# Kernel tuning notes

Hardware: AMD Instinct MI355X
Metric: run time of the kernel (lower is better)

## Reference

```python
import jax, jax.numpy as jnp
import numpy as np


def _wkv(time_decay, time_first, k, v):
    # time_decay, time_first: [C]; k, v: [B, T, C]
    w = -jnp.exp(time_decay)  # per-channel decay (negative)
    u = time_first
    B, T, C = k.shape
    aa = jnp.zeros((B, C), dtype=k.dtype)
    bb = jnp.zeros((B, C), dtype=k.dtype)
    pp = jnp.full((B, C), -1e38, dtype=k.dtype)  # running max exponent

    def step(carry, kv_t):
        aa, bb, pp = carry
        kt, vt = kv_t  # [B, C] each
        # output with bonus u for current token
        ww = u + kt
        q = jnp.maximum(pp, ww)
        e1 = jnp.exp(pp - q)
        e2 = jnp.exp(ww - q)
        y_t = (e1 * aa + e2 * vt) / (e1 * bb + e2)
        # decayed state update
        ww2 = pp + w
        q2 = jnp.maximum(ww2, kt)
        e1b = jnp.exp(ww2 - q2)
        e2b = jnp.exp(kt - q2)
        new_carry = (e1b * aa + e2b * vt, e1b * bb + e2b, q2)
        return new_carry, y_t

    ks = jnp.transpose(k, (1, 0, 2))  # [T, B, C]
    vs = jnp.transpose(v, (1, 0, 2))
    _, ys = jax.lax.scan(step, (aa, bb, pp), (ks, vs))
    return jnp.transpose(ys, (1, 0, 2))  # [B, T, C]


def setup_inputs() -> dict:
    key = jax.random.key(0)
    k1, k2, k3, k4 = jax.random.split(key, 4)
    B, T, C = 8, 1024, 2048
    return {
        "batch_size": B,
        "seq_len": T,
        "embedding_dim": C,
        "time_decay": jax.random.normal(k1, (C,), dtype=jnp.float32),
        "time_first": jax.random.normal(k2, (C,), dtype=jnp.float32),
        "k": jax.random.normal(k3, (B, T, C), dtype=jnp.float32),
        "v": jax.random.normal(k4, (B, T, C), dtype=jnp.float32),
    }


def reference(batch_size, seq_len, embedding_dim, time_decay, time_first, k, v):
    assert seq_len <= 1024  # T_max
    return _wkv(time_decay, time_first, k, v)
```

## Files before the change

kernel.cpp:

```cpp
#include <hip/hip_runtime.h>


#define T_FIX  1024
#define NCH    64
#define CHL    (T_FIX / NCH)
#define BATCH  8
#define SBATCH 8
#define L2E    1.4426950408889634f

__device__ __forceinline__ void wkv_step2(float& aa, float& bb, float& pp,
                                          float w2, float k2, float vt)
{
    float ww2 = pp + w2;
    float q2  = fmaxf(ww2, k2);
    float e1  = exp2f(ww2 - q2);
    float e2  = exp2f(k2 - q2);
    aa = fmaf(e1, aa, e2 * vt);
    bb = fmaf(e1, bb, e2);
    pp = q2;
}

#define F4TOA(a, f) { a[0] = (f).x; a[1] = (f).y; a[2] = (f).z; a[3] = (f).w; }

__global__ __launch_bounds__(256)
void wkv_states(const float* __restrict__ td,
                const float* __restrict__ k,
                const float* __restrict__ v,
                float* __restrict__ aa_s,
                float* __restrict__ bb_s,
                float* __restrict__ pp_s,
                int B, int C)
{
    const int C4  = C >> 2;
    int gid = blockIdx.x * blockDim.x + threadIdx.x;
    if (gid >= B * NCH * C4) return;
    int c4  = gid % C4;
    int rem = gid / C4;
    int j   = rem % NCH;
    int b   = rem / NCH;
    int c   = c4 << 2;

    float4 tdv = *(const float4*)(td + c);
    float w2[4] = { -__expf(tdv.x) * L2E, -__expf(tdv.y) * L2E,
                    -__expf(tdv.z) * L2E, -__expf(tdv.w) * L2E };

    const size_t base = ((size_t)b * T_FIX + (size_t)j * CHL) * C + c;
    const float* kp = k + base;
    const float* vp = v + base;

    float aa[4] = {0.f, 0.f, 0.f, 0.f};
    float bb[4] = {0.f, 0.f, 0.f, 0.f};
    float pp[4] = {-1e38f, -1e38f, -1e38f, -1e38f};

    for (int tb = 0; tb < CHL; tb += BATCH) {
        float4 kb[BATCH], vb[BATCH];
        #pragma unroll
        for (int i = 0; i < BATCH; ++i) {
            kb[i] = *(const float4*)(kp + (size_t)(tb + i) * C);
            vb[i] = *(const float4*)(vp + (size_t)(tb + i) * C);
        }
        #pragma unroll
        for (int i = 0; i < BATCH; ++i) {
            float ka[4], va[4];
            F4TOA(ka, kb[i]); F4TOA(va, vb[i]);
            #pragma unroll
            for (int cc = 0; cc < 4; ++cc)
                wkv_step2(aa[cc], bb[cc], pp[cc], w2[cc], ka[cc] * L2E, va[cc]);
        }
    }

    size_t sidx = ((size_t)j * B + b) * C + c;
    *(float4*)(aa_s + sidx) = make_float4(aa[0], aa[1], aa[2], aa[3]);
    *(float4*)(bb_s + sidx) = make_float4(bb[0], bb[1], bb[2], bb[3]);
    *(float4*)(pp_s + sidx) = make_float4(pp[0], pp[1], pp[2], pp[3]);
}

__global__ __launch_bounds__(256)
void wkv_scan(const float* __restrict__ td,
              float* __restrict__ aa_s,
              float* __restrict__ bb_s,
              float* __restrict__ pp_s,
              int B, int C)
{
    const int C4 = C >> 2;
    int gid = blockIdx.x * blockDim.x + threadIdx.x;
    if (gid >= B * C4) return;
    int c4 = gid % C4;
    int b  = gid / C4;
    int c  = c4 << 2;

    float4 tdv = *(const float4*)(td + c);
    float wL[4] = { -__expf(tdv.x) * (L2E * (float)CHL),
                    -__expf(tdv.y) * (L2E * (float)CHL),
                    -__expf(tdv.z) * (L2E * (float)CHL),
                    -__expf(tdv.w) * (L2E * (float)CHL) };

    float aa[4] = {0.f, 0.f, 0.f, 0.f};
    float bb[4] = {0.f, 0.f, 0.f, 0.f};
    float pp[4] = {-1e38f, -1e38f, -1e38f, -1e38f};

    for (int jb = 0; jb < NCH; jb += SBATCH) {
        float4 ca4[SBATCH], cb4[SBATCH], cm4[SBATCH];
        #pragma unroll
        for (int i = 0; i < SBATCH; ++i) {
            size_t sidx = ((size_t)(jb + i) * B + b) * C + c;
            ca4[i] = *(const float4*)(aa_s + sidx);
            cb4[i] = *(const float4*)(bb_s + sidx);
            cm4[i] = *(const float4*)(pp_s + sidx);
        }
        #pragma unroll
        for (int i = 0; i < SBATCH; ++i) {
            size_t sidx = ((size_t)(jb + i) * B + b) * C + c;
            *(float4*)(aa_s + sidx) = make_float4(aa[0], aa[1], aa[2], aa[3]);
            *(float4*)(bb_s + sidx) = make_float4(bb[0], bb[1], bb[2], bb[3]);
            *(float4*)(pp_s + sidx) = make_float4(pp[0], pp[1], pp[2], pp[3]);
            float ca[4], cb[4], cm[4];
            F4TOA(ca, ca4[i]); F4TOA(cb, cb4[i]); F4TOA(cm, cm4[i]);
            #pragma unroll
            for (int cc = 0; cc < 4; ++cc) {
                float ppd = pp[cc] + wL[cc];
                float pn  = fmaxf(ppd, cm[cc]);
                float ea  = exp2f(ppd - pn);
                float eb  = exp2f(cm[cc] - pn);
                aa[cc] = fmaf(ea, aa[cc], eb * ca[cc]);
                bb[cc] = fmaf(ea, bb[cc], eb * cb[cc]);
                pp[cc] = pn;
            }
        }
    }
}

__global__ __launch_bounds__(256)
void wkv_emit(const float* __restrict__ td,
              const float* __restrict__ tf,
              const float* __restrict__ k,
              const float* __restrict__ v,
              const float* __restrict__ aa_s,
              const float* __restrict__ bb_s,
              const float* __restrict__ pp_s,
              float* __restrict__ y,
              int B, int C)
{
    const int C4  = C >> 2;
    int gid = blockIdx.x * blockDim.x + threadIdx.x;
    if (gid >= B * NCH * C4) return;
    int c4  = gid % C4;
    int rem = gid / C4;
    int j   = rem % NCH;
    int b   = rem / NCH;
    int c   = c4 << 2;

    float4 tdv = *(const float4*)(td + c);
    float4 tfv = *(const float4*)(tf + c);
    float w2[4] = { -__expf(tdv.x) * L2E, -__expf(tdv.y) * L2E,
                    -__expf(tdv.z) * L2E, -__expf(tdv.w) * L2E };
    float u2[4] = { tfv.x * L2E, tfv.y * L2E, tfv.z * L2E, tfv.w * L2E };

    size_t sidx = ((size_t)j * B + b) * C + c;
    float4 a4 = *(const float4*)(aa_s + sidx);
    float4 b4 = *(const float4*)(bb_s + sidx);
    float4 p4 = *(const float4*)(pp_s + sidx);
    float aa[4], bb[4], pp[4];
    F4TOA(aa, a4); F4TOA(bb, b4); F4TOA(pp, p4);

    const size_t base = ((size_t)b * T_FIX + (size_t)j * CHL) * C + c;
    const float* kp = k + base;
    const float* vp = v + base;
    float*       yp = y + base;

    for (int tb = 0; tb < CHL; tb += BATCH) {
        float4 kb[BATCH], vb[BATCH];
        #pragma unroll
        for (int i = 0; i < BATCH; ++i) {
            kb[i] = *(const float4*)(kp + (size_t)(tb + i) * C);
            vb[i] = *(const float4*)(vp + (size_t)(tb + i) * C);
        }
        #pragma unroll
        for (int i = 0; i < BATCH; ++i) {
            float ka[4], va[4], ya[4];
            F4TOA(ka, kb[i]); F4TOA(va, vb[i]);
            #pragma unroll
            for (int cc = 0; cc < 4; ++cc) {
                float k2 = ka[cc] * L2E;
                float ww = u2[cc] + k2;
                float q  = fmaxf(pp[cc], ww);
                float e1 = exp2f(pp[cc] - q);
                float e2 = exp2f(ww - q);
                ya[cc] = __fdividef(fmaf(e1, aa[cc], e2 * va[cc]),
                                    fmaf(e1, bb[cc], e2));
                wkv_step2(aa[cc], bb[cc], pp[cc], w2[cc], k2, va[cc]);
            }
            *(float4*)(yp + (size_t)(tb + i) * C) = make_float4(ya[0], ya[1], ya[2], ya[3]);
        }
    }
}

extern "C" void kernel_launch(void* const* d_in, const int* in_sizes, int n_in,
                              void* d_out, int out_size, void* d_ws, size_t ws_size,
                              hipStream_t stream)
{
    const float* td = (const float*)d_in[3];
    const float* tf = (const float*)d_in[4];
    const float* k  = (const float*)d_in[5];
    const float* v  = (const float*)d_in[6];
    float*       y  = (float*)d_out;

    const int C   = in_sizes[3];
    const int BTC = in_sizes[5];
    const int B   = BTC / (T_FIX * C);

    const size_t N = (size_t)B * C * NCH;
    float* aa_s = (float*)d_ws;
    float* bb_s = aa_s + N;
    float* pp_s = bb_s + N;

    const int block = 256;

    const int threadsA = B * NCH * (C >> 2);
    const int gridA    = (threadsA + block - 1) / block;

    const int threadsS = B * (C >> 2);
    const int gridS    = (threadsS + block - 1) / block;

    wkv_states<<<gridA, block, 0, stream>>>(td, k, v, aa_s, bb_s, pp_s, B, C);
    wkv_scan  <<<gridS, block, 0, stream>>>(td, aa_s, bb_s, pp_s, B, C);
    wkv_emit  <<<gridA, block, 0, stream>>>(td, tf, k, v, aa_s, bb_s, pp_s, y, B, C);
}
```

Measured before the change: 232.0 us.

## Fuse chunked WKV into one kernel with in-block shared-memory prefix scan

Merges the three kernels (chunk states, serial cross-chunk scan, emit) into one. Each 512-thread block owns one batch and a 32-channel tile across all 64 time chunks. The chunk states go into shared memory and are combined with a Hillis-Steele log-step scan that uses the decay scaled by the chunk distance. This removes the global-memory round trip of the chunk states, the serial 64-step scan kernel and two launch gaps. In exchange it adds block-wide barriers and leaves k and v read twice, now within one block where they may stay in cache.

```diff
diff --git a/kernel.cpp b/kernel.cpp
--- a/kernel.cpp
+++ b/kernel.cpp
@@ -5,8 +5,12 @@
 #define NCH    64
 #define CHL    (T_FIX / NCH)
 #define BATCH  8
-#define SBATCH 8
+#define CTILE  32
+#define CGT    (CTILE / 4)
+#define NTHR   (NCH * CGT)
 #define L2E    1.4426950408889634f
+
+#define F4TOA(a, f) { a[0] = (f).x; a[1] = (f).y; a[2] = (f).z; a[3] = (f).w; }
 
 __device__ __forceinline__ void wkv_step2(float& aa, float& bb, float& pp,
                                           float w2, float k2, float vt)
@@ -20,33 +24,36 @@
     pp = q2;
 }
 
-#define F4TOA(a, f) { a[0] = (f).x; a[1] = (f).y; a[2] = (f).z; a[3] = (f).w; }
+__global__ __launch_bounds__(NTHR, 4)
+void wkv_fused(const float* __restrict__ td,
+               const float* __restrict__ tf,
+               const float* __restrict__ k,
+               const float* __restrict__ v,
+               float* __restrict__ y,
+               int B, int C)
+{
+    __shared__ float4 a_s[NTHR];
+    __shared__ float4 b_s[NTHR];
+    __shared__ float4 p_s[NTHR];
 
-__global__ __launch_bounds__(256)
-void wkv_states(const float* __restrict__ td,
-                const float* __restrict__ k,
-                const float* __restrict__ v,
-                float* __restrict__ aa_s,
-                float* __restrict__ bb_s,
-                float* __restrict__ pp_s,
-                int B, int C)
-{
-    const int C4  = C >> 2;
-    int gid = blockIdx.x * blockDim.x + threadIdx.x;
-    if (gid >= B * NCH * C4) return;
-    int c4  = gid % C4;
-    int rem = gid / C4;
-    int j   = rem % NCH;
-    int b   = rem / NCH;
-    int c   = c4 << 2;
+    const int tid = threadIdx.x;
+    const int cg  = tid & (CGT - 1);
+    const int j   = tid >> 3;
+
+    const int tiles = C / CTILE;
+    const int b  = blockIdx.x / tiles;
+    const int c  = (blockIdx.x % tiles) * CTILE + (cg << 2);
 
     float4 tdv = *(const float4*)(td + c);
+    float4 tfv = *(const float4*)(tf + c);
     float w2[4] = { -__expf(tdv.x) * L2E, -__expf(tdv.y) * L2E,
                     -__expf(tdv.z) * L2E, -__expf(tdv.w) * L2E };
+    float u2[4] = { tfv.x * L2E, tfv.y * L2E, tfv.z * L2E, tfv.w * L2E };
 
     const size_t base = ((size_t)b * T_FIX + (size_t)j * CHL) * C + c;
     const float* kp = k + base;
     const float* vp = v + base;
+    float*       yp = y + base;
 
     float aa[4] = {0.f, 0.f, 0.f, 0.f};
     float bb[4] = {0.f, 0.f, 0.f, 0.f};
@@ -69,104 +76,50 @@
         }
     }
 
-    size_t sidx = ((size_t)j * B + b) * C + c;
-    *(float4*)(aa_s + sidx) = make_float4(aa[0], aa[1], aa[2], aa[3]);
-    *(float4*)(bb_s + sidx) = make_float4(bb[0], bb[1], bb[2], bb[3]);
-    *(float4*)(pp_s + sidx) = make_float4(pp[0], pp[1], pp[2], pp[3]);
-}
+    a_s[tid] = make_float4(aa[0], aa[1], aa[2], aa[3]);
+    b_s[tid] = make_float4(bb[0], bb[1], bb[2], bb[3]);
+    p_s[tid] = make_float4(pp[0], pp[1], pp[2], pp[3]);
+    __syncthreads();
 
-__global__ __launch_bounds__(256)
-void wkv_scan(const float* __restrict__ td,
-              float* __restrict__ aa_s,
-              float* __restrict__ bb_s,
-              float* __restrict__ pp_s,
-              int B, int C)
-{
-    const int C4 = C >> 2;
-    int gid = blockIdx.x * blockDim.x + threadIdx.x;
-    if (gid >= B * C4) return;
-    int c4 = gid % C4;
-    int b  = gid / C4;
-    int c  = c4 << 2;
-
-    float4 tdv = *(const float4*)(td + c);
-    float wL[4] = { -__expf(tdv.x) * (L2E * (float)CHL),
-                    -__expf(tdv.y) * (L2E * (float)CHL),
-                    -__expf(tdv.z) * (L2E * (float)CHL),
-                    -__expf(tdv.w) * (L2E * (float)CHL) };
-
-    float aa[4] = {0.f, 0.f, 0.f, 0.f};
-    float bb[4] = {0.f, 0.f, 0.f, 0.f};
-    float pp[4] = {-1e38f, -1e38f, -1e38f, -1e38f};
-
-    for (int jb = 0; jb < NCH; jb += SBATCH) {
-        float4 ca4[SBATCH], cb4[SBATCH], cm4[SBATCH];
-        #pragma unroll
-        for (int i = 0; i < SBATCH; ++i) {
-            size_t sidx = ((size_t)(jb + i) * B + b) * C + c;
-            ca4[i] = *(const float4*)(aa_s + sidx);
-            cb4[i] = *(const float4*)(bb_s + sidx);
-            cm4[i] = *(const float4*)(pp_s + sidx);
+    #pragma unroll
+    for (int d = 1; d < NCH; d <<= 1) {
+        float pa[4], pb[4], pm[4];
+        const bool act = (j >= d);
+        if (act) {
+            float4 xa = a_s[tid - CGT * d];
+            float4 xb = b_s[tid - CGT * d];
+            float4 xp = p_s[tid - CGT * d];
+            F4TOA(pa, xa); F4TOA(pb, xb); F4TOA(pm, xp);
         }
-        #pragma unroll
-        for (int i = 0; i < SBATCH; ++i) {
-            size_t sidx = ((size_t)(jb + i) * B + b) * C + c;
-            *(float4*)(aa_s + sidx) = make_float4(aa[0], aa[1], aa[2], aa[3]);
-            *(float4*)(bb_s + sidx) = make_float4(bb[0], bb[1], bb[2], bb[3]);
-            *(float4*)(pp_s + sidx) = make_float4(pp[0], pp[1], pp[2], pp[3]);
-            float ca[4], cb[4], cm[4];
-            F4TOA(ca, ca4[i]); F4TOA(cb, cb4[i]); F4TOA(cm, cm4[i]);
+        __syncthreads();
+        if (act) {
+            const float Ld = (float)(d * CHL);
             #pragma unroll
             for (int cc = 0; cc < 4; ++cc) {
-                float ppd = pp[cc] + wL[cc];
-                float pn  = fmaxf(ppd, cm[cc]);
+                float ppd = fmaf(Ld, w2[cc], pm[cc]);
+                float pn  = fmaxf(ppd, pp[cc]);
                 float ea  = exp2f(ppd - pn);
-                float eb  = exp2f(cm[cc] - pn);
-                aa[cc] = fmaf(ea, aa[cc], eb * ca[cc]);
-                bb[cc] = fmaf(ea, bb[cc], eb * cb[cc]);
+                float eb  = exp2f(pp[cc] - pn);
+                aa[cc] = fmaf(ea, pa[cc], eb * aa[cc]);
+                bb[cc] = fmaf(ea, pb[cc], eb * bb[cc]);
                 pp[cc] = pn;
             }
+            a_s[tid] = make_float4(aa[0], aa[1], aa[2], aa[3]);
+            b_s[tid] = make_float4(bb[0], bb[1], bb[2], bb[3]);
+            p_s[tid] = make_float4(pp[0], pp[1], pp[2], pp[3]);
         }
+        __syncthreads();
     }
-}
 
-__global__ __launch_bounds__(256)
-void wkv_emit(const float* __restrict__ td,
-              const float* __restrict__ tf,
-              const float* __restrict__ k,
-              const float* __restrict__ v,
-              const float* __restrict__ aa_s,
-              const float* __restrict__ bb_s,
-              const float* __restrict__ pp_s,
-              float* __restrict__ y,
-              int B, int C)
-{
-    const int C4  = C >> 2;
-    int gid = blockIdx.x * blockDim.x + threadIdx.x;
-    if (gid >= B * NCH * C4) return;
-    int c4  = gid % C4;
-    int rem = gid / C4;
-    int j   = rem % NCH;
-    int b   = rem / NCH;
-    int c   = c4 << 2;
-
-    float4 tdv = *(const float4*)(td + c);
-    float4 tfv = *(const float4*)(tf + c);
-    float w2[4] = { -__expf(tdv.x) * L2E, -__expf(tdv.y) * L2E,
-                    -__expf(tdv.z) * L2E, -__expf(tdv.w) * L2E };
-    float u2[4] = { tfv.x * L2E, tfv.y * L2E, tfv.z * L2E, tfv.w * L2E };
-
-    size_t sidx = ((size_t)j * B + b) * C + c;
-    float4 a4 = *(const float4*)(aa_s + sidx);
-    float4 b4 = *(const float4*)(bb_s + sidx);
-    float4 p4 = *(const float4*)(pp_s + sidx);
-    float aa[4], bb[4], pp[4];
-    F4TOA(aa, a4); F4TOA(bb, b4); F4TOA(pp, p4);
-
-    const size_t base = ((size_t)b * T_FIX + (size_t)j * CHL) * C + c;
-    const float* kp = k + base;
-    const float* vp = v + base;
-    float*       yp = y + base;
+    if (j > 0) {
+        float4 xa = a_s[tid - CGT];
+        float4 xb = b_s[tid - CGT];
+        float4 xp = p_s[tid - CGT];
+        F4TOA(aa, xa); F4TOA(bb, xb); F4TOA(pp, xp);
+    } else {
+        #pragma unroll
+        for (int cc = 0; cc < 4; ++cc) { aa[cc] = 0.f; bb[cc] = 0.f; pp[cc] = -1e38f; }
+    }
 
     for (int tb = 0; tb < CHL; tb += BATCH) {
         float4 kb[BATCH], vb[BATCH];
@@ -209,20 +162,6 @@
     const int BTC = in_sizes[5];
     const int B   = BTC / (T_FIX * C);
 
-    const size_t N = (size_t)B * C * NCH;
-    float* aa_s = (float*)d_ws;
-    float* bb_s = aa_s + N;
-    float* pp_s = bb_s + N;
-
-    const int block = 256;
-
-    const int threadsA = B * NCH * (C >> 2);
-    const int gridA    = (threadsA + block - 1) / block;
-
-    const int threadsS = B * (C >> 2);
-    const int gridS    = (threadsS + block - 1) / block;
-
-    wkv_states<<<gridA, block, 0, stream>>>(td, k, v, aa_s, bb_s, pp_s, B, C);
-    wkv_scan  <<<gridS, block, 0, stream>>>(td, aa_s, bb_s, pp_s, B, C);
-    wkv_emit  <<<gridA, block, 0, stream>>>(td, tf, k, v, aa_s, bb_s, pp_s, y, B, C);
+    const int grid = B * (C / CTILE);
+    wkv_fused<<<grid, NTHR, 0, stream>>>(td, tf, k, v, y, B, C);
 }
```

New measurement: 260.9 us. +12.4%, slower.
